# Optimization experiments

Hardware: AMD Instinct MI355X
Metric: run time of the kernel (lower is better)

Reference implementation:

```python
import jax, jax.numpy as jnp
import numpy as np

N = 50000        # nodes
E = 1_600_000    # edges (avg degree 32)
G = 512          # graphs
F_IN = 9         # node features
H = 64           # hidden dim
ED = 1           # edge feature dim


def _lin(k, fo, fi):
    w = jax.random.normal(k, (fo, fi), jnp.float32) * (1.0 / np.sqrt(fi))
    b = jnp.zeros((fo,), jnp.float32)
    return w, b


def setup_inputs() -> dict:
    key = jax.random.key(0)
    ks = jax.random.split(key, 16)
    x = jax.random.normal(ks[0], (N, F_IN), jnp.float32)
    edge_index = jax.random.randint(ks[1], (2, E), 0, N, dtype=jnp.int64)
    edge_attr = jax.random.normal(ks[2], (E, ED), jnp.float32)
    batch = jnp.sort(jax.random.randint(ks[3], (N,), 0, G, dtype=jnp.int64))
    B_total = jax.random.uniform(ks[4], (G,), jnp.float32) * 100.0
    terminal_mask = jax.random.randint(ks[5], (N,), 0, 2, dtype=jnp.int32)
    c_cost = jax.random.uniform(ks[6], (N,), jnp.float32)
    # conv1: edge lin (ED->F_IN), nn = Linear(F_IN,H), Linear(H,H)
    e1_w, e1_b = _lin(ks[7], F_IN, ED)
    w1a, b1a = _lin(ks[8], H, F_IN)
    w1b, b1b = _lin(ks[9], H, H)
    # conv2: edge lin (ED->H), nn = Linear(H,H), Linear(H,H)
    e2_w, e2_b = _lin(ks[10], H, ED)
    w2a, b2a = _lin(ks[11], H, H)
    w2b, b2b = _lin(ks[12], H, H)
    # readout: Linear(H,H//2), Linear(H//2,1)
    wr1, br1 = _lin(ks[13], H // 2, H)
    wr2, br2 = _lin(ks[14], 1, H // 2)
    return dict(x=x, edge_index=edge_index, edge_attr=edge_attr, batch=batch,
                B_total=B_total, terminal_mask=terminal_mask, c_cost=c_cost,
                e1_w=e1_w, e1_b=e1_b, w1a=w1a, b1a=b1a, w1b=w1b, b1b=b1b,
                e2_w=e2_w, e2_b=e2_b, w2a=w2a, b2a=b2a, w2b=w2b, b2b=b2b,
                wr1=wr1, br1=br1, wr2=wr2, br2=br2)


def _gine(x, src, dst, edge_attr, ew, eb, wa, ba, wb, bb):
    # GINEConv (eps=0): nn(x + sum_j relu(x_j + W_e e_ji))
    e = edge_attr @ ew.T + eb                    # [E, F]
    m = jax.nn.relu(x[src] + e)                  # [E, F] gather + edge fuse
    aggr = jax.ops.segment_sum(m, dst, num_segments=N)  # scatter-add -> [N, F]
    h = x + aggr
    h = jax.nn.relu(h @ wa.T + ba)
    h = jax.nn.relu(h @ wb.T + bb)
    return h


def reference(x, edge_index, edge_attr, batch, B_total, terminal_mask, c_cost,
              e1_w, e1_b, w1a, b1a, w1b, b1b,
              e2_w, e2_b, w2a, b2a, w2b, b2b,
              wr1, br1, wr2, br2):
    src, dst = edge_index[0], edge_index[1]
    h = _gine(x, src, dst, edge_attr, e1_w, e1_b, w1a, b1a, w1b, b1b)
    h = _gine(h, src, dst, edge_attr, e2_w, e2_b, w2a, b2a, w2b, b2b)
    pi_raw = jax.nn.sigmoid((jax.nn.relu(h @ wr1.T + br1) @ wr2.T + br2))[:, 0]
    pi_raw = pi_raw * (1.0 - terminal_mask.astype(jnp.float32))
    node_expenses = pi_raw * c_cost
    total_expenses = jax.ops.segment_sum(node_expenses, batch, num_segments=G)
    ratio = jnp.minimum(B_total[batch] / (total_expenses[batch] + 1e-12), 1.0)
    return pi_raw * ratio
```

## Files before the change

kernel.cpp:

```cpp
#include <hip/hip_runtime.h>
#include <hip/hip_fp16.h>
#include <math.h>

#define N_NODES 50000
#define N_EDGES 1600000
#define N_GRAPHS 512
#define F_IN 9
#define H 64
#define N_BUCKETS ((N_NODES + 255) >> 8)
#define EPB 4096
#define N_SBLK ((N_EDGES + EPB - 1) / EPB)
#define FINE_CAP 10240

typedef _Float16 f16x8 __attribute__((ext_vector_type(8)));
typedef float f32x4 __attribute__((ext_vector_type(4)));

__device__ __forceinline__ void pack_weights_body(
        const float* __restrict__ w1a, const float* __restrict__ w1b,
        const float* __restrict__ w2a, const float* __restrict__ w2b,
        const float* __restrict__ wr1,
        __half* __restrict__ pk1Ah, __half* __restrict__ pk1Al,
        __half* __restrict__ pk1Bh, __half* __restrict__ pk1Bl,
        __half* __restrict__ pkAh, __half* __restrict__ pkAl,
        __half* __restrict__ pkBh, __half* __restrict__ pkBl,
        __half* __restrict__ pkRh, __half* __restrict__ pkRl) {
    int t = threadIdx.x;
    for (int i = t; i < 2048; i += 256) {
        int j = i & 7, l = (i >> 3) & 63, tt = i >> 9;
        int q = l >> 4, n = l & 15;
        int k = q * 8 + j;
        float v = (k < F_IN) ? w1a[(tt * 16 + n) * F_IN + k] : 0.f;
        __half h = __float2half(v);
        pk1Ah[i] = h; pk1Al[i] = __float2half(v - __half2float(h));
    }
    for (int i = t; i < 4096; i += 256) {
        int j = i & 7, l = (i >> 3) & 63, c = (i >> 9) & 1, tt = i >> 10;
        int q = l >> 4, n = l & 15;
        int src = (tt * 16 + n) * H + c * 32 + q * 8 + j;
        float v1 = w1b[src], wa = w2a[src], wb = w2b[src];
        __half h1 = __float2half(v1), ah = __float2half(wa), bh = __float2half(wb);
        pk1Bh[i] = h1; pk1Bl[i] = __float2half(v1 - __half2float(h1));
        pkAh[i] = ah; pkAl[i] = __float2half(wa - __half2float(ah));
        pkBh[i] = bh; pkBl[i] = __float2half(wb - __half2float(bh));
    }
    for (int i = t; i < 2048; i += 256) {
        int j = i & 7, l = (i >> 3) & 63, c = (i >> 9) & 1, tt = i >> 10;
        int q = l >> 4, n = l & 15;
        float wr = wr1[(tt * 16 + n) * H + c * 32 + q * 8 + j];
        __half rh = __float2half(wr);
        pkRh[i] = rh; pkRl[i] = __float2half(wr - __half2float(rh));
    }
}

__global__ void bucket_scatter(const int* __restrict__ ei,
                               const float* __restrict__ ea,
                               int* __restrict__ bnext,
                               uint2* __restrict__ ebuk,
                               const float* __restrict__ w1a,
                               const float* __restrict__ w1b,
                               const float* __restrict__ w2a,
                               const float* __restrict__ w2b,
                               const float* __restrict__ wr1,
                               __half* pk1Ah, __half* pk1Al,
                               __half* pk1Bh, __half* pk1Bl,
                               __half* pkAh, __half* pkAl,
                               __half* pkBh, __half* pkBl,
                               __half* pkRh, __half* pkRl) {
    if (blockIdx.x == 0) {
        pack_weights_body(w1a, w1b, w2a, w2b, wr1, pk1Ah, pk1Al, pk1Bh, pk1Bl,
                          pkAh, pkAl, pkBh, pkBl, pkRh, pkRl);
        return;
    }
    __shared__ int cnt[N_BUCKETS];
    __shared__ int gbase[N_BUCKETS];
    for (int i = threadIdx.x; i < N_BUCKETS; i += 256) cnt[i] = 0;
    __syncthreads();
    int base = (blockIdx.x - 1) * EPB;
    int rk[16];
#pragma unroll
    for (int j = 0; j < 16; ++j) {
        int e = base + j * 256 + threadIdx.x;
        rk[j] = -1;
        if (e < N_EDGES) {
            int d = ei[N_EDGES + e];
            int b = d >> 8;
            int r = atomicAdd(&cnt[b], 1);
            rk[j] = (b << 21) | ((d & 255) << 13) | r;
        }
    }
    __syncthreads();
    for (int i = threadIdx.x; i < N_BUCKETS; i += 256)
        gbase[i] = cnt[i] ? atomicAdd(&bnext[i], cnt[i]) : 0;
    __syncthreads();
#pragma unroll
    for (int j = 0; j < 16; ++j) {
        if (rk[j] < 0) continue;
        int e = base + j * 256 + threadIdx.x;
        int b = rk[j] >> 21, dl = (rk[j] >> 13) & 255, r = rk[j] & 8191;
        int slot = gbase[b] + r;
        if (slot >= FINE_CAP) continue;
        unsigned pay = ((unsigned)ei[e] << 16) |
                       (unsigned)__half_as_ushort(__float2half(ea[e]));
        ebuk[(size_t)b * FINE_CAP + slot] = make_uint2(pay, (unsigned)dl);
    }
}

__global__ void __launch_bounds__(256)
bucket_fine(const uint2* __restrict__ ebuk,
            const int* __restrict__ bnext,
            unsigned* __restrict__ ep4,
            int* __restrict__ starts, int* __restrict__ deg) {
    __shared__ unsigned sorted[FINE_CAP];
    __shared__ int cntN[256], offN[256], nxtN[256];
    __shared__ int wsum[4];
    int b = blockIdx.x;
    int base = b * FINE_CAP;
    int count = bnext[b];
    if (count > FINE_CAP) count = FINE_CAP;
    int tid = threadIdx.x;
    cntN[tid] = 0;
    __syncthreads();
    for (int i = tid; i < count; i += 256)
        atomicAdd(&cntN[ebuk[base + i].y], 1);
    __syncthreads();
    int lane = tid & 63, wid = tid >> 6;
    int v = cntN[tid], incl = v;
#pragma unroll
    for (int off = 1; off < 64; off <<= 1) {
        int t = __shfl_up(incl, off, 64);
        if (lane >= off) incl += t;
    }
    if (lane == 63) wsum[wid] = incl;
    __syncthreads();
    int woff = 0;
    for (int w = 0; w < wid; ++w) woff += wsum[w];
    int excl = woff + incl - v;
    offN[tid] = excl;
    nxtN[tid] = 0;
    int n = (b << 8) + tid;
    if (n < N_NODES) { starts[n] = base + excl; deg[n] = v; }
    __syncthreads();
    for (int i = tid; i < count; i += 256) {
        uint2 e = ebuk[base + i];
        int r = atomicAdd(&nxtN[e.y], 1);
        sorted[offN[e.y] + r] = e.x;
    }
    __syncthreads();
    for (int i = tid; i < count; i += 256)
        ep4[base + i] = sorted[i];
}

#define UNPACK_ATTR(P) __half2float(__ushort_as_half((unsigned short)((P) & 0xffffu)))

__global__ void agg1_kernel(const float* __restrict__ x,
                            const int* __restrict__ starts,
                            const int* __restrict__ deg,
                            const unsigned* __restrict__ ep4,
                            const float* __restrict__ e1w,
                            const float* __restrict__ e1b,
                            float* __restrict__ xs) {
    int n = blockIdx.x * (blockDim.x >> 6) + (threadIdx.x >> 6);
    int lane = threadIdx.x & 63;
    if (n >= N_NODES) return;
    int slot = lane >> 4;
    int f = lane & 15;
    int s0 = starts[n], dg = deg[n];
    bool act = f < F_IN;
    float wf = act ? e1w[f] : 0.f;
    float bf = act ? e1b[f] : 0.f;
    float acc = 0.f;
    int j = slot;
    for (; j + 12 < dg; j += 16) {
        unsigned pa = ep4[s0 + j];
        unsigned pb = ep4[s0 + j + 4];
        unsigned pc = ep4[s0 + j + 8];
        unsigned pd = ep4[s0 + j + 12];
        float xa_ = act ? x[(pa >> 16) * F_IN + f] : 0.f;
        float xb_ = act ? x[(pb >> 16) * F_IN + f] : 0.f;
        float xc_ = act ? x[(pc >> 16) * F_IN + f] : 0.f;
        float xd_ = act ? x[(pd >> 16) * F_IN + f] : 0.f;
        if (act) {
            acc += fmaxf(xa_ + UNPACK_ATTR(pa) * wf + bf, 0.f)
                 + fmaxf(xb_ + UNPACK_ATTR(pb) * wf + bf, 0.f)
                 + fmaxf(xc_ + UNPACK_ATTR(pc) * wf + bf, 0.f)
                 + fmaxf(xd_ + UNPACK_ATTR(pd) * wf + bf, 0.f);
        }
    }
    for (; j < dg; j += 4) {
        unsigned p = ep4[s0 + j];
        float xv = act ? x[(p >> 16) * F_IN + f] : 0.f;
        float m = xv + UNPACK_ATTR(p) * wf + bf;
        acc += act ? fmaxf(m, 0.f) : 0.f;
    }
    acc += __shfl_xor(acc, 16, 64);
    acc += __shfl_xor(acc, 32, 64);
    if (lane < 32)
        xs[n * 32 + lane] = (lane < F_IN) ? x[n * F_IN + lane] + acc : 0.f;
}

__device__ __forceinline__ void split8(const float* __restrict__ v,
                                       f16x8& hi, f16x8& lo) {
#pragma unroll
    for (int j = 0; j < 8; ++j) {
        _Float16 h = (_Float16)v[j];
        hi[j] = h;
        lo[j] = (_Float16)(v[j] - (float)h);
    }
}

#define TILE3(C, A0H, A0L, A1H, A1L, PH, PL, T) do {                          \
        f16x8 b0h = *(const f16x8*)((PH) + (((T) * 2 + 0) * 64 + lane) * 8);  \
        f16x8 b0l = *(const f16x8*)((PL) + (((T) * 2 + 0) * 64 + lane) * 8);  \
        f16x8 b1h = *(const f16x8*)((PH) + (((T) * 2 + 1) * 64 + lane) * 8);  \
        f16x8 b1l = *(const f16x8*)((PL) + (((T) * 2 + 1) * 64 + lane) * 8);  \
        C = __builtin_amdgcn_mfma_f32_16x16x32_f16(A0H, b0h, C, 0, 0, 0);     \
        C = __builtin_amdgcn_mfma_f32_16x16x32_f16(A0L, b0h, C, 0, 0, 0);     \
        C = __builtin_amdgcn_mfma_f32_16x16x32_f16(A0H, b0l, C, 0, 0, 0);     \
        C = __builtin_amdgcn_mfma_f32_16x16x32_f16(A1H, b1h, C, 0, 0, 0);     \
        C = __builtin_amdgcn_mfma_f32_16x16x32_f16(A1L, b1h, C, 0, 0, 0);     \
        C = __builtin_amdgcn_mfma_f32_16x16x32_f16(A1H, b1l, C, 0, 0, 0);     \
    } while (0)

__global__ void node1_kernel(const float* __restrict__ xs,
                             const __half* __restrict__ pk1Ah, const __half* __restrict__ pk1Al,
                             const float* __restrict__ b1a,
                             const __half* __restrict__ pk1Bh, const __half* __restrict__ pk1Bl,
                             const float* __restrict__ b1b,
                             __half* __restrict__ h1lo,
                             __half* __restrict__ h1hi) {
    __shared__ float hbuf[4][16][68];
    int wv = threadIdx.x >> 6;
    int lane = threadIdx.x & 63;
    int gwave = blockIdx.x * 4 + wv;
    bool active = gwave < (N_NODES / 16);
    int base = active ? gwave * 16 : 0;
    int m = lane & 15, q = lane >> 4;
    const _Float16* pAh = (const _Float16*)pk1Ah;
    const _Float16* pAl = (const _Float16*)pk1Al;
    const _Float16* pBh = (const _Float16*)pk1Bh;
    const _Float16* pBl = (const _Float16*)pk1Bl;

    f16x8 ah, al;
    split8(xs + (size_t)(base + m) * 32 + q * 8, ah, al);
#pragma unroll
    for (int t = 0; t < 4; ++t) {
        f32x4 c = {0.f, 0.f, 0.f, 0.f};
        f16x8 bh = *(const f16x8*)(pAh + (t * 64 + lane) * 8);
        f16x8 bl = *(const f16x8*)(pAl + (t * 64 + lane) * 8);
        c = __builtin_amdgcn_mfma_f32_16x16x32_f16(ah, bh, c, 0, 0, 0);
        c = __builtin_amdgcn_mfma_f32_16x16x32_f16(al, bh, c, 0, 0, 0);
        c = __builtin_amdgcn_mfma_f32_16x16x32_f16(ah, bl, c, 0, 0, 0);
        float bias = b1a[t * 16 + m];
#pragma unroll
        for (int r = 0; r < 4; ++r)
            hbuf[wv][q * 4 + r][t * 16 + m] = fmaxf(c[r] + bias, 0.f);
    }
    __syncthreads();
    f16x8 a0h, a0l, a1h, a1l;
    split8(&hbuf[wv][m][q * 8], a0h, a0l);
    split8(&hbuf[wv][m][32 + q * 8], a1h, a1l);
    float tmp[4][4];
#pragma unroll
    for (int t = 0; t < 4; ++t) {
        f32x4 c = {0.f, 0.f, 0.f, 0.f};
        TILE3(c, a0h, a0l, a1h, a1l, pBh, pBl, t);
        float bias = b1b[t * 16 + m];
#pragma unroll
        for (int r = 0; r < 4; ++r)
            tmp[t][r] = fmaxf(c[r] + bias, 0.f);
    }
    __syncthreads();
#pragma unroll
    for (int t = 0; t < 4; ++t)
#pragma unroll
        for (int r = 0; r < 4; ++r)
            hbuf[wv][q * 4 + r][t * 16 + m] = tmp[t][r];
    __syncthreads();
    if (active) {
        int nn = lane >> 2, part = lane & 3;
        f16x8 vlo, vhi;
        const float* rlo = &hbuf[wv][nn][part * 8];
        const float* rhi = &hbuf[wv][nn][32 + part * 8];
#pragma unroll
        for (int j = 0; j < 8; ++j) {
            vlo[j] = (_Float16)rlo[j];
            vhi[j] = (_Float16)rhi[j];
        }
        *(f16x8*)(h1lo + (size_t)(base + nn) * 32 + part * 8) = vlo;
        *(f16x8*)(h1hi + (size_t)(base + nn) * 32 + part * 8) = vhi;
    }
}

__global__ void aggphase_kernel(const __half* __restrict__ harr,
                                const int* __restrict__ starts,
                                const int* __restrict__ deg,
                                const unsigned* __restrict__ ep4,
                                const float* __restrict__ ew,
                                const float* __restrict__ eb,
                                float* __restrict__ htot, int foff) {
    int n = blockIdx.x * (blockDim.x >> 6) + (threadIdx.x >> 6);
    int lane = threadIdx.x & 63;
    if (n >= N_NODES) return;
    int half = lane >> 5;
    int fh = lane & 31;
    int s0 = starts[n], dg = deg[n];
    const unsigned* ep = ep4 + s0;
    float wf = ew[fh], bf = eb[fh];
    float acc = 0.f;
    int j = 0;
#define EDGE1(P, V) acc += fmaxf((V) + UNPACK_ATTR(P) * wf + bf, 0.f)
    for (; j + 16 <= dg; j += 16) {
        unsigned p0 = ep[j +  0 + half], p1 = ep[j +  2 + half];
        unsigned p2 = ep[j +  4 + half], p3 = ep[j +  6 + half];
        unsigned p4 = ep[j +  8 + half], p5 = ep[j + 10 + half];
        unsigned p6 = ep[j + 12 + half], p7 = ep[j + 14 + half];
        float v0 = __half2float(harr[(p0 >> 16) * 32 + fh]);
        float v1 = __half2float(harr[(p1 >> 16) * 32 + fh]);
        float v2 = __half2float(harr[(p2 >> 16) * 32 + fh]);
        float v3 = __half2float(harr[(p3 >> 16) * 32 + fh]);
        float v4 = __half2float(harr[(p4 >> 16) * 32 + fh]);
        float v5 = __half2float(harr[(p5 >> 16) * 32 + fh]);
        float v6 = __half2float(harr[(p6 >> 16) * 32 + fh]);
        float v7 = __half2float(harr[(p7 >> 16) * 32 + fh]);
        EDGE1(p0, v0); EDGE1(p1, v1); EDGE1(p2, v2); EDGE1(p3, v3);
        EDGE1(p4, v4); EDGE1(p5, v5); EDGE1(p6, v6); EDGE1(p7, v7);
    }
    for (; j + 2 <= dg; j += 2) {
        unsigned p = ep[j + half];
        float v = __half2float(harr[(p >> 16) * 32 + fh]);
        EDGE1(p, v);
    }
    if (j < dg && half == 0) {
        unsigned p = ep[j];
        float v = __half2float(harr[(p >> 16) * 32 + fh]);
        EDGE1(p, v);
    }
#undef EDGE1
    acc += __shfl_xor(acc, 32, 64);
    if (half == 0) {
        float h1v = __half2float(harr[n * 32 + fh]);
        htot[(size_t)n * 64 + foff + fh] = h1v + acc;
    }
}

__global__ void node2_kernel(const float* __restrict__ htot,
                             const __half* __restrict__ pkAh, const __half* __restrict__ pkAl,
                             const float* __restrict__ b2a,
                             const __half* __restrict__ pkBh, const __half* __restrict__ pkBl,
                             const float* __restrict__ b2b,
                             const __half* __restrict__ pkRh, const __half* __restrict__ pkRl,
                             const float* __restrict__ br1,
                             const float* __restrict__ wr2,
                             const float* __restrict__ br2,
                             const int* __restrict__ term,
                             float* __restrict__ pi) {
    __shared__ float hbuf[4][16][68];
    int wv = threadIdx.x >> 6;
    int lane = threadIdx.x & 63;
    int gwave = blockIdx.x * 4 + wv;
    bool active = gwave < (N_NODES / 16);
    int base = active ? gwave * 16 : 0;
    int m = lane & 15, q = lane >> 4;
    const _Float16* pAh = (const _Float16*)pkAh;
    const _Float16* pAl = (const _Float16*)pkAl;
    const _Float16* pBh = (const _Float16*)pkBh;
    const _Float16* pBl = (const _Float16*)pkBl;
    const _Float16* pRh = (const _Float16*)pkRh;
    const _Float16* pRl = (const _Float16*)pkRl;

    f16x8 a0h, a0l, a1h, a1l;
    {
        const float* hrow = htot + (size_t)(base + m) * 64;
        split8(hrow + q * 8, a0h, a0l);
        split8(hrow + 32 + q * 8, a1h, a1l);
    }
#pragma unroll
    for (int t = 0; t < 4; ++t) {
        f32x4 c = {0.f, 0.f, 0.f, 0.f};
        TILE3(c, a0h, a0l, a1h, a1l, pAh, pAl, t);
        float bias = b2a[t * 16 + m];
#pragma unroll
        for (int r = 0; r < 4; ++r)
            hbuf[wv][q * 4 + r][t * 16 + m] = fmaxf(c[r] + bias, 0.f);
    }
    __syncthreads();
    split8(&hbuf[wv][m][q * 8], a0h, a0l);
    split8(&hbuf[wv][m][32 + q * 8], a1h, a1l);
    float tmp[4][4];
#pragma unroll
    for (int t = 0; t < 4; ++t) {
        f32x4 c = {0.f, 0.f, 0.f, 0.f};
        TILE3(c, a0h, a0l, a1h, a1l, pBh, pBl, t);
        float bias = b2b[t * 16 + m];
#pragma unroll
        for (int r = 0; r < 4; ++r)
            tmp[t][r] = fmaxf(c[r] + bias, 0.f);
    }
    __syncthreads();
#pragma unroll
    for (int t = 0; t < 4; ++t)
#pragma unroll
        for (int r = 0; r < 4; ++r)
            hbuf[wv][q * 4 + r][t * 16 + m] = tmp[t][r];
    __syncthreads();
    split8(&hbuf[wv][m][q * 8], a0h, a0l);
    split8(&hbuf[wv][m][32 + q * 8], a1h, a1l);
    float partial[4] = {0.f, 0.f, 0.f, 0.f};
#pragma unroll
    for (int t = 0; t < 2; ++t) {
        f32x4 c = {0.f, 0.f, 0.f, 0.f};
        TILE3(c, a0h, a0l, a1h, a1l, pRh, pRl, t);
        float bias = br1[t * 16 + m];
        float wv2 = wr2[t * 16 + m];
#pragma unroll
        for (int r = 0; r < 4; ++r)
            partial[r] += fmaxf(c[r] + bias, 0.f) * wv2;
    }
#pragma unroll
    for (int off = 1; off < 16; off <<= 1) {
        partial[0] += __shfl_xor(partial[0], off, 64);
        partial[1] += __shfl_xor(partial[1], off, 64);
        partial[2] += __shfl_xor(partial[2], off, 64);
        partial[3] += __shfl_xor(partial[3], off, 64);
    }
    if (active && m == 0) {
#pragma unroll
        for (int r = 0; r < 4; ++r) {
            int n = base + q * 4 + r;
            float z = partial[r] + br2[0];
            float sig = 1.f / (1.f + expf(-z));
            pi[n] = sig * (1.f - (float)term[n]);
        }
    }
}

__global__ void te_kernel(const float* __restrict__ pi,
                          const float* __restrict__ ccost,
                          const int* __restrict__ batch,
                          float* __restrict__ te) {
    __shared__ float tg[N_GRAPHS];
    for (int i = threadIdx.x; i < N_GRAPHS; i += 1024) tg[i] = 0.f;
    __syncthreads();
    int n = blockIdx.x * 1024 + threadIdx.x;
    if (n < N_NODES) atomicAdd(&tg[batch[n]], pi[n] * ccost[n]);
    __syncthreads();
    for (int i = threadIdx.x; i < N_GRAPHS; i += 1024)
        if (tg[i] != 0.f) atomicAdd(&te[i], tg[i]);
}

__global__ void final_kernel(const float* __restrict__ pi,
                             const int* __restrict__ batch,
                             const float* __restrict__ Btot,
                             const float* __restrict__ te,
                             float* __restrict__ out) {
    int n = blockIdx.x * blockDim.x + threadIdx.x;
    if (n >= N_NODES) return;
    int b = batch[n];
    float ratio = fminf(Btot[b] / (te[b] + 1e-12f), 1.f);
    out[n] = pi[n] * ratio;
}

extern "C" void kernel_launch(void* const* d_in, const int* in_sizes, int n_in,
                              void* d_out, int out_size, void* d_ws, size_t ws_size,
                              hipStream_t stream) {
    const float* x     = (const float*)d_in[0];
    const int*   ei    = (const int*)d_in[1];
    const float* ea    = (const float*)d_in[2];
    const int*   batch = (const int*)d_in[3];
    const float* Btot  = (const float*)d_in[4];
    const int*   term  = (const int*)d_in[5];
    const float* ccost = (const float*)d_in[6];
    const float* e1w   = (const float*)d_in[7];
    const float* e1b   = (const float*)d_in[8];
    const float* w1a   = (const float*)d_in[9];
    const float* b1a   = (const float*)d_in[10];
    const float* w1b   = (const float*)d_in[11];
    const float* b1b   = (const float*)d_in[12];
    const float* e2w   = (const float*)d_in[13];
    const float* e2b   = (const float*)d_in[14];
    const float* w2a   = (const float*)d_in[15];
    const float* b2a   = (const float*)d_in[16];
    const float* w2b   = (const float*)d_in[17];
    const float* b2b   = (const float*)d_in[18];
    const float* wr1   = (const float*)d_in[19];
    const float* br1   = (const float*)d_in[20];
    const float* wr2   = (const float*)d_in[21];
    const float* br2   = (const float*)d_in[22];

    char* p = (char*)d_ws;
    int*      bnext  = (int*)p;      p += sizeof(int)      * 256;
    float*    te     = (float*)p;    p += sizeof(float)    * N_GRAPHS;
    int*      starts = (int*)p;      p += sizeof(int)      * N_NODES;
    int*      deg    = (int*)p;      p += sizeof(int)      * N_NODES;
    p = (char*)(((size_t)p + 15) & ~(size_t)15);
    uint2*    ebuk   = (uint2*)p;    p += sizeof(uint2)    * (size_t)N_BUCKETS * FINE_CAP;
    unsigned* ep4    = (unsigned*)p; p += sizeof(unsigned) * (size_t)N_BUCKETS * FINE_CAP;
    __half*   h1lo   = (__half*)p;   p += sizeof(__half)   * (size_t)N_NODES * 32;
    __half*   h1hi   = (__half*)p;   p += sizeof(__half)   * (size_t)N_NODES * 32;
    float*    htot   = (float*)p;    p += sizeof(float)    * (size_t)N_NODES * 64;
    float*    xs     = (float*)p;    p += sizeof(float)    * (size_t)N_NODES * 32;
    float*    pi     = (float*)p;    p += sizeof(float)    * N_NODES;
    __half*   pk1Ah  = (__half*)p;   p += sizeof(__half)   * 2048;
    __half*   pk1Al  = (__half*)p;   p += sizeof(__half)   * 2048;
    __half*   pk1Bh  = (__half*)p;   p += sizeof(__half)   * 4096;
    __half*   pk1Bl  = (__half*)p;   p += sizeof(__half)   * 4096;
    __half*   pkAh   = (__half*)p;   p += sizeof(__half)   * 4096;
    __half*   pkAl   = (__half*)p;   p += sizeof(__half)   * 4096;
    __half*   pkBh   = (__half*)p;   p += sizeof(__half)   * 4096;
    __half*   pkBl   = (__half*)p;   p += sizeof(__half)   * 4096;
    __half*   pkRh   = (__half*)p;   p += sizeof(__half)   * 2048;
    __half*   pkRl   = (__half*)p;   p += sizeof(__half)   * 2048;
    float*    out    = (float*)d_out;

    hipMemsetAsync(d_ws, 0, sizeof(int) * 256 + sizeof(float) * N_GRAPHS, stream);

    bucket_scatter<<<1 + N_SBLK, 256, 0, stream>>>(ei, ea, bnext, ebuk,
                                                   w1a, w1b, w2a, w2b, wr1,
                                                   pk1Ah, pk1Al, pk1Bh, pk1Bl,
                                                   pkAh, pkAl, pkBh, pkBl, pkRh, pkRl);
    bucket_fine<<<N_BUCKETS, 256, 0, stream>>>(ebuk, bnext, ep4, starts, deg);
    agg1_kernel<<<(N_NODES + 3) / 4, 256, 0, stream>>>(x, starts, deg, ep4, e1w, e1b, xs);
    node1_kernel<<<(N_NODES / 16 + 3) / 4, 256, 0, stream>>>(xs, pk1Ah, pk1Al, b1a,
                                                             pk1Bh, pk1Bl, b1b,
                                                             h1lo, h1hi);
    aggphase_kernel<<<(N_NODES + 3) / 4, 256, 0, stream>>>(h1lo, starts, deg, ep4,
                                                           e2w, e2b, htot, 0);
    aggphase_kernel<<<(N_NODES + 3) / 4, 256, 0, stream>>>(h1hi, starts, deg, ep4,
                                                           e2w + 32, e2b + 32, htot, 32);
    node2_kernel<<<(N_NODES / 16 + 3) / 4, 256, 0, stream>>>(htot,
                                                             pkAh, pkAl, b2a,
                                                             pkBh, pkBl, b2b,
                                                             pkRh, pkRl, br1,
                                                             wr2, br2, term, pi);
    te_kernel<<<(N_NODES + 1023) / 1024, 1024, 0, stream>>>(pi, ccost, batch, te);
    final_kernel<<<(N_NODES + 255) / 256, 256, 0, stream>>>(pi, batch, Btot, te, out);
}
```

Before: 261.9 us.

## Merge split-half edge aggregation into one pass and fuse graph-expense reduction

The two aggregation passes over the lo/hi feature halves become one kernel that reads an interleaved 64-wide fp16 node array, so each wave gathers a full 128-byte row per edge and the edge list is read once instead of twice. The per-graph expense sum moves into node2 as global atomics, which removes the te kernel launch and the extra pass over pi. In exchange, every node now does a global atomicAdd where the old kernel pre-reduced in shared memory first, which can add contention on the 512 graph accumulators.

```diff
diff --git a/kernel.cpp b/kernel.cpp
--- a/kernel.cpp
+++ b/kernel.cpp
@@ -226,8 +226,7 @@
                              const float* __restrict__ b1a,
                              const __half* __restrict__ pk1Bh, const __half* __restrict__ pk1Bl,
                              const float* __restrict__ b1b,
-                             __half* __restrict__ h1lo,
-                             __half* __restrict__ h1hi) {
+                             __half* __restrict__ h1) {
     __shared__ float hbuf[4][16][68];
     int wv = threadIdx.x >> 6;
     int lane = threadIdx.x & 63;
@@ -286,61 +285,58 @@
             vlo[j] = (_Float16)rlo[j];
             vhi[j] = (_Float16)rhi[j];
         }
-        *(f16x8*)(h1lo + (size_t)(base + nn) * 32 + part * 8) = vlo;
-        *(f16x8*)(h1hi + (size_t)(base + nn) * 32 + part * 8) = vhi;
-    }
-}
-
-__global__ void aggphase_kernel(const __half* __restrict__ harr,
-                                const int* __restrict__ starts,
-                                const int* __restrict__ deg,
-                                const unsigned* __restrict__ ep4,
-                                const float* __restrict__ ew,
-                                const float* __restrict__ eb,
-                                float* __restrict__ htot, int foff) {
+        *(f16x8*)(h1 + (size_t)(base + nn) * 64 + part * 8) = vlo;
+        *(f16x8*)(h1 + (size_t)(base + nn) * 64 + 32 + part * 8) = vhi;
+    }
+}
+
+__global__ void aggphase2_kernel(const __half* __restrict__ h1,
+                                 const int* __restrict__ starts,
+                                 const int* __restrict__ deg,
+                                 const unsigned* __restrict__ ep4,
+                                 const float* __restrict__ ew,
+                                 const float* __restrict__ eb,
+                                 float* __restrict__ htot) {
     int n = blockIdx.x * (blockDim.x >> 6) + (threadIdx.x >> 6);
     int lane = threadIdx.x & 63;
     if (n >= N_NODES) return;
-    int half = lane >> 5;
-    int fh = lane & 31;
     int s0 = starts[n], dg = deg[n];
     const unsigned* ep = ep4 + s0;
-    float wf = ew[fh], bf = eb[fh];
+    float wf = ew[lane], bf = eb[lane];
     float acc = 0.f;
+#define EDGE1(P, V) acc += fmaxf((V) + UNPACK_ATTR(P) * wf + bf, 0.f)
     int j = 0;
-#define EDGE1(P, V) acc += fmaxf((V) + UNPACK_ATTR(P) * wf + bf, 0.f)
-    for (; j + 16 <= dg; j += 16) {
-        unsigned p0 = ep[j +  0 + half], p1 = ep[j +  2 + half];
-        unsigned p2 = ep[j +  4 + half], p3 = ep[j +  6 + half];
-        unsigned p4 = ep[j +  8 + half], p5 = ep[j + 10 + half];
-        unsigned p6 = ep[j + 12 + half], p7 = ep[j + 14 + half];
-        float v0 = __half2float(harr[(p0 >> 16) * 32 + fh]);
-        float v1 = __half2float(harr[(p1 >> 16) * 32 + fh]);
-        float v2 = __half2float(harr[(p2 >> 16) * 32 + fh]);
-        float v3 = __half2float(harr[(p3 >> 16) * 32 + fh]);
-        float v4 = __half2float(harr[(p4 >> 16) * 32 + fh]);
-        float v5 = __half2float(harr[(p5 >> 16) * 32 + fh]);
-        float v6 = __half2float(harr[(p6 >> 16) * 32 + fh]);
-        float v7 = __half2float(harr[(p7 >> 16) * 32 + fh]);
+    for (; j + 8 <= dg; j += 8) {
+        unsigned p0 = ep[j + 0], p1 = ep[j + 1], p2 = ep[j + 2], p3 = ep[j + 3];
+        unsigned p4 = ep[j + 4], p5 = ep[j + 5], p6 = ep[j + 6], p7 = ep[j + 7];
+        float v0 = __half2float(h1[(size_t)(p0 >> 16) * 64 + lane]);
+        float v1 = __half2float(h1[(size_t)(p1 >> 16) * 64 + lane]);
+        float v2 = __half2float(h1[(size_t)(p2 >> 16) * 64 + lane]);
+        float v3 = __half2float(h1[(size_t)(p3 >> 16) * 64 + lane]);
+        float v4 = __half2float(h1[(size_t)(p4 >> 16) * 64 + lane]);
+        float v5 = __half2float(h1[(size_t)(p5 >> 16) * 64 + lane]);
+        float v6 = __half2float(h1[(size_t)(p6 >> 16) * 64 + lane]);
+        float v7 = __half2float(h1[(size_t)(p7 >> 16) * 64 + lane]);
         EDGE1(p0, v0); EDGE1(p1, v1); EDGE1(p2, v2); EDGE1(p3, v3);
         EDGE1(p4, v4); EDGE1(p5, v5); EDGE1(p6, v6); EDGE1(p7, v7);
     }
-    for (; j + 2 <= dg; j += 2) {
-        unsigned p = ep[j + half];
-        float v = __half2float(harr[(p >> 16) * 32 + fh]);
+    if (j + 4 <= dg) {
+        unsigned p0 = ep[j + 0], p1 = ep[j + 1], p2 = ep[j + 2], p3 = ep[j + 3];
+        float v0 = __half2float(h1[(size_t)(p0 >> 16) * 64 + lane]);
+        float v1 = __half2float(h1[(size_t)(p1 >> 16) * 64 + lane]);
+        float v2 = __half2float(h1[(size_t)(p2 >> 16) * 64 + lane]);
+        float v3 = __half2float(h1[(size_t)(p3 >> 16) * 64 + lane]);
+        EDGE1(p0, v0); EDGE1(p1, v1); EDGE1(p2, v2); EDGE1(p3, v3);
+        j += 4;
+    }
+    for (; j < dg; ++j) {
+        unsigned p = ep[j];
+        float v = __half2float(h1[(size_t)(p >> 16) * 64 + lane]);
         EDGE1(p, v);
     }
-    if (j < dg && half == 0) {
-        unsigned p = ep[j];
-        float v = __half2float(harr[(p >> 16) * 32 + fh]);
-        EDGE1(p, v);
-    }
 #undef EDGE1
-    acc += __shfl_xor(acc, 32, 64);
-    if (half == 0) {
-        float h1v = __half2float(harr[n * 32 + fh]);
-        htot[(size_t)n * 64 + foff + fh] = h1v + acc;
-    }
+    float self = __half2float(h1[(size_t)n * 64 + lane]);
+    htot[(size_t)n * 64 + lane] = self + acc;
 }
 
 __global__ void node2_kernel(const float* __restrict__ htot,
@@ -353,7 +349,10 @@
                              const float* __restrict__ wr2,
                              const float* __restrict__ br2,
                              const int* __restrict__ term,
-                             float* __restrict__ pi) {
+                             const int* __restrict__ batch,
+                             const float* __restrict__ ccost,
+                             float* __restrict__ pi,
+                             float* __restrict__ te) {
     __shared__ float hbuf[4][16][68];
     int wv = threadIdx.x >> 6;
     int lane = threadIdx.x & 63;
@@ -429,23 +428,12 @@
             int n = base + q * 4 + r;
             float z = partial[r] + br2[0];
             float sig = 1.f / (1.f + expf(-z));
-            pi[n] = sig * (1.f - (float)term[n]);
+            float pv = sig * (1.f - (float)term[n]);
+            pi[n] = pv;
+            float contrib = pv * ccost[n];
+            if (contrib != 0.f) atomicAdd(&te[batch[n]], contrib);
         }
     }
-}
-
-__global__ void te_kernel(const float* __restrict__ pi,
-                          const float* __restrict__ ccost,
-                          const int* __restrict__ batch,
-                          float* __restrict__ te) {
-    __shared__ float tg[N_GRAPHS];
-    for (int i = threadIdx.x; i < N_GRAPHS; i += 1024) tg[i] = 0.f;
-    __syncthreads();
-    int n = blockIdx.x * 1024 + threadIdx.x;
-    if (n < N_NODES) atomicAdd(&tg[batch[n]], pi[n] * ccost[n]);
-    __syncthreads();
-    for (int i = threadIdx.x; i < N_GRAPHS; i += 1024)
-        if (tg[i] != 0.f) atomicAdd(&te[i], tg[i]);
 }
 
 __global__ void final_kernel(const float* __restrict__ pi,
@@ -495,8 +483,7 @@
     p = (char*)(((size_t)p + 15) & ~(size_t)15);
     uint2*    ebuk   = (uint2*)p;    p += sizeof(uint2)    * (size_t)N_BUCKETS * FINE_CAP;
     unsigned* ep4    = (unsigned*)p; p += sizeof(unsigned) * (size_t)N_BUCKETS * FINE_CAP;
-    __half*   h1lo   = (__half*)p;   p += sizeof(__half)   * (size_t)N_NODES * 32;
-    __half*   h1hi   = (__half*)p;   p += sizeof(__half)   * (size_t)N_NODES * 32;
+    __half*   h1     = (__half*)p;   p += sizeof(__half)   * (size_t)N_NODES * 64;
     float*    htot   = (float*)p;    p += sizeof(float)    * (size_t)N_NODES * 64;
     float*    xs     = (float*)p;    p += sizeof(float)    * (size_t)N_NODES * 32;
     float*    pi     = (float*)p;    p += sizeof(float)    * N_NODES;
@@ -521,17 +508,14 @@
     bucket_fine<<<N_BUCKETS, 256, 0, stream>>>(ebuk, bnext, ep4, starts, deg);
     agg1_kernel<<<(N_NODES + 3) / 4, 256, 0, stream>>>(x, starts, deg, ep4, e1w, e1b, xs);
     node1_kernel<<<(N_NODES / 16 + 3) / 4, 256, 0, stream>>>(xs, pk1Ah, pk1Al, b1a,
-                                                             pk1Bh, pk1Bl, b1b,
-                                                             h1lo, h1hi);
-    aggphase_kernel<<<(N_NODES + 3) / 4, 256, 0, stream>>>(h1lo, starts, deg, ep4,
-                                                           e2w, e2b, htot, 0);
-    aggphase_kernel<<<(N_NODES + 3) / 4, 256, 0, stream>>>(h1hi, starts, deg, ep4,
-                                                           e2w + 32, e2b + 32, htot, 32);
+                                                             pk1Bh, pk1Bl, b1b, h1);
+    aggphase2_kernel<<<(N_NODES + 3) / 4, 256, 0, stream>>>(h1, starts, deg, ep4,
+                                                            e2w, e2b, htot);
     node2_kernel<<<(N_NODES / 16 + 3) / 4, 256, 0, stream>>>(htot,
                                                              pkAh, pkAl, b2a,
                                                              pkBh, pkBl, b2b,
                                                              pkRh, pkRl, br1,
-                                                             wr2, br2, term, pi);
-    te_kernel<<<(N_NODES + 1023) / 1024, 1024, 0, stream>>>(pi, ccost, batch, te);
+                                                             wr2, br2, term,
+                                                             batch, ccost, pi, te);
     final_kernel<<<(N_NODES + 255) / 256, 256, 0, stream>>>(pi, batch, Btot, te, out);
 }
```

After: 254.2 us. 1.03x faster.
